# Optimization experiments

Hardware: AMD Instinct MI355X
Metric: run time of the kernel (lower is better)

The kernel has to match this reference:

```python
import jax, jax.numpy as jnp
import numpy as np

MEM = 2048

def _linear_params(key, scale):
    kw, kb = jax.random.split(key)
    W = jax.random.uniform(kw, (MEM, MEM), jnp.float32, -scale, scale)
    b = jax.random.uniform(kb, (MEM,), jnp.float32, -scale, scale)
    return W, b

def setup_inputs() -> dict:
    key = jax.random.key(0)
    ks = jax.random.split(key, 18)
    scale = 1.0 / np.sqrt(MEM)
    inp = {
        'lc': jax.random.normal(ks[0], (1, MEM), jnp.float32),
        'lh': jax.random.normal(ks[1], (1, MEM), jnp.float32),
        'rc': jax.random.normal(ks[2], (1, MEM), jnp.float32),
        'rh': jax.random.normal(ks[3], (1, MEM), jnp.float32),
        'S': jax.random.normal(ks[4], (1, MEM), jnp.float32),
        'w': jax.random.normal(ks[5], (1, MEM), jnp.float32),
    }
    names = ['Wh', 'Us', 'ma', 'ilh', 'irh', 'lflh', 'lfrh', 'rflh', 'rfrh', 'ulh', 'urh']
    for i, n in enumerate(names):
        W, b = _linear_params(ks[6 + i], scale)
        inp[n + '_w'] = W
        inp[n + '_b'] = b
    return inp

def _lin(x, W, b):
    return x @ W.T + b

def reference(lc, lh, rc, rh, S, w,
              Wh_w, Wh_b, Us_w, Us_b, ma_w, ma_b,
              ilh_w, ilh_b, irh_w, irh_b,
              lflh_w, lflh_b, lfrh_w, lfrh_b,
              rflh_w, rflh_b, rfrh_w, rfrh_b,
              ulh_w, ulh_b, urh_w, urh_b):
    # attention scoring over the two children
    m_left = jnp.tanh(_lin(lh, Wh_w, Wh_b) + _lin(S, Us_w, Us_b)).squeeze()   # [MEM]
    m_right = jnp.tanh(_lin(rh, Wh_w, Wh_b) + _lin(S, Us_w, Us_b)).squeeze()  # [MEM]
    exp_left = w @ m_left[:, None]    # [1,1]
    exp_right = w @ m_right[:, None]  # [1,1]
    denom = exp_left + exp_right
    left_alpha = exp_left / denom
    right_alpha = exp_right / denom
    # attention-weighted child hidden states
    la = jnp.tanh(_lin(left_alpha * lh, ma_w, ma_b))   # [1,MEM]
    ra = jnp.tanh(_lin(right_alpha * rh, ma_w, ma_b))  # [1,MEM]
    # tree-LSTM gates
    i = jax.nn.sigmoid(_lin(la, ilh_w, ilh_b) + _lin(ra, irh_w, irh_b))
    lf = jax.nn.sigmoid(_lin(la, lflh_w, lflh_b) + _lin(ra, lfrh_w, lfrh_b))
    rf = jax.nn.sigmoid(_lin(la, rflh_w, rflh_b) + _lin(ra, rfrh_w, rfrh_b))
    update = jnp.tanh(_lin(la, ulh_w, ulh_b) + _lin(ra, urh_w, urh_b))
    c = i * update + lf * lc + rf * rc
    h = jnp.tanh(c)
    return (c, h)
```

## Files before the change

### kernel.cpp

```cpp
#include <hip/hip_runtime.h>
#include <hip/hip_bf16.h>
#include <math.h>

#define MEM 2048
#define NF4 (MEM / 4)

__device__ __forceinline__ float wave_reduce(float v) {
#pragma unroll
    for (int off = 32; off > 0; off >>= 1)
        v += __shfl_down(v, off, 64);
    return v;
}

__device__ __forceinline__ float sigmoidf_(float x) {
    return 1.0f / (1.0f + expf(-x));
}

__global__ __launch_bounds__(256) void
k1_score(const float* __restrict__ lh, const float* __restrict__ rh,
         const float* __restrict__ S,  const float* __restrict__ w,
         const float* __restrict__ Wh_w, const float* __restrict__ Wh_b,
         const float* __restrict__ Us_w, const float* __restrict__ Us_b,
         const float* __restrict__ ma_w,
         float* __restrict__ pl, float* __restrict__ pr,
         float* __restrict__ eacc)
{
    __shared__ __align__(16) float s_lh[MEM];
    __shared__ __align__(16) float s_rh[MEM];
    __shared__ __align__(16) float s_S[MEM];
    __shared__ float s_e[8];

    const int tid = threadIdx.x;
    for (int i = tid; i < MEM; i += 256) {
        s_lh[i] = lh[i];
        s_rh[i] = rh[i];
        s_S[i]  = S[i];
    }
    __syncthreads();

    const int wave = tid >> 6;
    const int lane = tid & 63;
    const int row  = blockIdx.x * 4 + wave;

    const float4* __restrict__ wr = (const float4*)(Wh_w + (size_t)row * MEM);
    const float4* __restrict__ ur = (const float4*)(Us_w + (size_t)row * MEM);
    const float4* __restrict__ mr = (const float4*)(ma_w + (size_t)row * MEM);
    const float4* l4 = (const float4*)s_lh;
    const float4* r4 = (const float4*)s_rh;
    const float4* s4 = (const float4*)s_S;

    float awl = 0.f, awr = 0.f, aus = 0.f, aml = 0.f, amr = 0.f;
#pragma unroll 2
    for (int it = 0; it < NF4 / 64; ++it) {
        const int idx = it * 64 + lane;
        const float4 wv = wr[idx];
        const float4 uv = ur[idx];
        const float4 mv = mr[idx];
        const float4 xl = l4[idx];
        const float4 xr = r4[idx];
        const float4 xs = s4[idx];
        awl += wv.x * xl.x + wv.y * xl.y + wv.z * xl.z + wv.w * xl.w;
        awr += wv.x * xr.x + wv.y * xr.y + wv.z * xr.z + wv.w * xr.w;
        aus += uv.x * xs.x + uv.y * xs.y + uv.z * xs.z + uv.w * xs.w;
        aml += mv.x * xl.x + mv.y * xl.y + mv.z * xl.z + mv.w * xl.w;
        amr += mv.x * xr.x + mv.y * xr.y + mv.z * xr.z + mv.w * xr.w;
    }
    awl = wave_reduce(awl);
    awr = wave_reduce(awr);
    aus = wave_reduce(aus);
    aml = wave_reduce(aml);
    amr = wave_reduce(amr);

    if (lane == 0) {
        const float us = aus + Us_b[row];
        const float ml = tanhf(awl + Wh_b[row] + us);
        const float mrv = tanhf(awr + Wh_b[row] + us);
        pl[row] = aml;
        pr[row] = amr;
        const float wj = w[row];
        s_e[wave]     = wj * ml;
        s_e[4 + wave] = wj * mrv;
    }
    __syncthreads();
    if (tid == 0) {
        atomicAdd(&eacc[0], s_e[0] + s_e[1] + s_e[2] + s_e[3]);
        atomicAdd(&eacc[1], s_e[4] + s_e[5] + s_e[6] + s_e[7]);
    }
}

__global__ __launch_bounds__(256) void
k2_gates(const float* __restrict__ lc, const float* __restrict__ rc,
         const float* __restrict__ pl, const float* __restrict__ pr,
         const float* __restrict__ eacc, const float* __restrict__ ma_b,
         const float* __restrict__ ilh_w,  const float* __restrict__ ilh_b,
         const float* __restrict__ irh_w,  const float* __restrict__ irh_b,
         const float* __restrict__ lflh_w, const float* __restrict__ lflh_b,
         const float* __restrict__ lfrh_w, const float* __restrict__ lfrh_b,
         const float* __restrict__ rflh_w, const float* __restrict__ rflh_b,
         const float* __restrict__ rfrh_w, const float* __restrict__ rfrh_b,
         const float* __restrict__ ulh_w,  const float* __restrict__ ulh_b,
         const float* __restrict__ urh_w,  const float* __restrict__ urh_b,
         float* __restrict__ out)
{
    __shared__ __align__(16) float s_la[MEM];
    __shared__ __align__(16) float s_ra[MEM];

    const int tid = threadIdx.x;
    const float el = eacc[0];
    const float er = eacc[1];
    const float denom = el + er;
    const float al = el / denom;
    const float ar = er / denom;

    for (int i = tid; i < MEM; i += 256) {
        const float mb = ma_b[i];
        s_la[i] = tanhf(al * pl[i] + mb);
        s_ra[i] = tanhf(ar * pr[i] + mb);
    }
    __syncthreads();

    const int wave = tid >> 6;
    const int lane = tid & 63;
    const int row  = blockIdx.x * 4 + wave;
    const size_t off = (size_t)row * MEM;

    const float4* __restrict__ il4  = (const float4*)(ilh_w  + off);
    const float4* __restrict__ ir4  = (const float4*)(irh_w  + off);
    const float4* __restrict__ lfl4 = (const float4*)(lflh_w + off);
    const float4* __restrict__ lfr4 = (const float4*)(lfrh_w + off);
    const float4* __restrict__ rfl4 = (const float4*)(rflh_w + off);
    const float4* __restrict__ rfr4 = (const float4*)(rfrh_w + off);
    const float4* __restrict__ ul4  = (const float4*)(ulh_w  + off);
    const float4* __restrict__ ur4  = (const float4*)(urh_w  + off);
    const float4* la4 = (const float4*)s_la;
    const float4* ra4 = (const float4*)s_ra;

    float ai = 0.f, bi = 0.f, alf = 0.f, blf = 0.f;
    float arf = 0.f, brf = 0.f, au = 0.f, bu = 0.f;
#pragma unroll 2
    for (int it = 0; it < NF4 / 64; ++it) {
        const int idx = it * 64 + lane;
        const float4 xa = la4[idx];
        const float4 xb = ra4[idx];
        float4 v;
        v = il4[idx];  ai  += v.x * xa.x + v.y * xa.y + v.z * xa.z + v.w * xa.w;
        v = ir4[idx];  bi  += v.x * xb.x + v.y * xb.y + v.z * xb.z + v.w * xb.w;
        v = lfl4[idx]; alf += v.x * xa.x + v.y * xa.y + v.z * xa.z + v.w * xa.w;
        v = lfr4[idx]; blf += v.x * xb.x + v.y * xb.y + v.z * xb.z + v.w * xb.w;
        v = rfl4[idx]; arf += v.x * xa.x + v.y * xa.y + v.z * xa.z + v.w * xa.w;
        v = rfr4[idx]; brf += v.x * xb.x + v.y * xb.y + v.z * xb.z + v.w * xb.w;
        v = ul4[idx];  au  += v.x * xa.x + v.y * xa.y + v.z * xa.z + v.w * xa.w;
        v = ur4[idx];  bu  += v.x * xb.x + v.y * xb.y + v.z * xb.z + v.w * xb.w;
    }

    const float gi  = wave_reduce(ai + bi);
    const float glf = wave_reduce(alf + blf);
    const float grf = wave_reduce(arf + brf);
    const float gu  = wave_reduce(au + bu);

    if (lane == 0) {
        const float ig  = sigmoidf_(gi  + ilh_b[row]  + irh_b[row]);
        const float lfg = sigmoidf_(glf + lflh_b[row] + lfrh_b[row]);
        const float rfg = sigmoidf_(grf + rflh_b[row] + rfrh_b[row]);
        const float ug  = tanhf(gu + ulh_b[row] + urh_b[row]);
        const float c = ig * ug + lfg * lc[row] + rfg * rc[row];
        out[row]       = c;
        out[MEM + row] = tanhf(c);
    }
}

extern "C" void kernel_launch(void* const* d_in, const int* in_sizes, int n_in,
                              void* d_out, int out_size, void* d_ws, size_t ws_size,
                              hipStream_t stream) {
    const float* lc = (const float*)d_in[0];
    const float* lh = (const float*)d_in[1];
    const float* rc = (const float*)d_in[2];
    const float* rh = (const float*)d_in[3];
    const float* S  = (const float*)d_in[4];
    const float* w  = (const float*)d_in[5];
    const float* Wh_w   = (const float*)d_in[6];   const float* Wh_b   = (const float*)d_in[7];
    const float* Us_w   = (const float*)d_in[8];   const float* Us_b   = (const float*)d_in[9];
    const float* ma_w   = (const float*)d_in[10];  const float* ma_b   = (const float*)d_in[11];
    const float* ilh_w  = (const float*)d_in[12];  const float* ilh_b  = (const float*)d_in[13];
    const float* irh_w  = (const float*)d_in[14];  const float* irh_b  = (const float*)d_in[15];
    const float* lflh_w = (const float*)d_in[16];  const float* lflh_b = (const float*)d_in[17];
    const float* lfrh_w = (const float*)d_in[18];  const float* lfrh_b = (const float*)d_in[19];
    const float* rflh_w = (const float*)d_in[20];  const float* rflh_b = (const float*)d_in[21];
    const float* rfrh_w = (const float*)d_in[22];  const float* rfrh_b = (const float*)d_in[23];
    const float* ulh_w  = (const float*)d_in[24];  const float* ulh_b  = (const float*)d_in[25];
    const float* urh_w  = (const float*)d_in[26];  const float* urh_b  = (const float*)d_in[27];

    float* out  = (float*)d_out;
    float* ws   = (float*)d_ws;
    float* eacc = ws;
    float* pl   = ws + 64;
    float* pr   = ws + 64 + MEM;

    hipMemsetAsync(eacc, 0, 2 * sizeof(float), stream);

    k1_score<<<MEM / 4, 256, 0, stream>>>(lh, rh, S, w, Wh_w, Wh_b, Us_w, Us_b,
                                          ma_w, pl, pr, eacc);

    k2_gates<<<MEM / 4, 256, 0, stream>>>(lc, rc, pl, pr, eacc, ma_b,
                                          ilh_w, ilh_b, irh_w, irh_b,
                                          lflh_w, lflh_b, lfrh_w, lfrh_b,
                                          rflh_w, rflh_b, rfrh_w, rfrh_b,
                                          ulh_w, ulh_b, urh_w, urh_b, out);
}
```

Before: 261.1 us.

## Use one block per row and replace atomics with per-row score buffers

Each weight row is now handled by a whole 256-thread block, up from one wave per row, and the launch uses 2048 blocks. The first kernel no longer stages the input vectors in shared memory and reads them straight from global/L2. Instead of accumulating attention scores with atomics after a memset, it writes per-row w*m values to a buffer. The second kernel reduces that buffer at the start of every block. This removes the memset launch and the atomic contention, and raises the number of in-flight memory requests for the bandwidth-bound GEMVs. The cost is redundant score reductions and tanh recomputation in every block, plus extra block-level reductions.

```diff
diff --git a/kernel.cpp b/kernel.cpp
--- a/kernel.cpp
+++ b/kernel.cpp
@@ -3,7 +3,12 @@
 #include <math.h>
 
 #define MEM 2048
+#define NT  256
 #define NF4 (MEM / 4)
+
+__device__ __forceinline__ float dot4(float4 a, float4 b) {
+    return a.x * b.x + a.y * b.y + a.z * b.z + a.w * b.w;
+}
 
 __device__ __forceinline__ float wave_reduce(float v) {
 #pragma unroll
@@ -16,54 +21,42 @@
     return 1.0f / (1.0f + expf(-x));
 }
 
-__global__ __launch_bounds__(256) void
+__global__ __launch_bounds__(NT) void
 k1_score(const float* __restrict__ lh, const float* __restrict__ rh,
          const float* __restrict__ S,  const float* __restrict__ w,
          const float* __restrict__ Wh_w, const float* __restrict__ Wh_b,
          const float* __restrict__ Us_w, const float* __restrict__ Us_b,
          const float* __restrict__ ma_w,
          float* __restrict__ pl, float* __restrict__ pr,
-         float* __restrict__ eacc)
+         float* __restrict__ wml, float* __restrict__ wmr)
 {
-    __shared__ __align__(16) float s_lh[MEM];
-    __shared__ __align__(16) float s_rh[MEM];
-    __shared__ __align__(16) float s_S[MEM];
-    __shared__ float s_e[8];
-
-    const int tid = threadIdx.x;
-    for (int i = tid; i < MEM; i += 256) {
-        s_lh[i] = lh[i];
-        s_rh[i] = rh[i];
-        s_S[i]  = S[i];
-    }
-    __syncthreads();
-
-    const int wave = tid >> 6;
-    const int lane = tid & 63;
-    const int row  = blockIdx.x * 4 + wave;
-
-    const float4* __restrict__ wr = (const float4*)(Wh_w + (size_t)row * MEM);
-    const float4* __restrict__ ur = (const float4*)(Us_w + (size_t)row * MEM);
-    const float4* __restrict__ mr = (const float4*)(ma_w + (size_t)row * MEM);
-    const float4* l4 = (const float4*)s_lh;
-    const float4* r4 = (const float4*)s_rh;
-    const float4* s4 = (const float4*)s_S;
+    __shared__ float s_red[4][5];
+
+    const int t   = threadIdx.x;
+    const int row = blockIdx.x;
+
+    const float4* __restrict__ wh4 = (const float4*)(Wh_w + (size_t)row * MEM);
+    const float4* __restrict__ us4 = (const float4*)(Us_w + (size_t)row * MEM);
+    const float4* __restrict__ ma4 = (const float4*)(ma_w + (size_t)row * MEM);
+    const float4* __restrict__ l4  = (const float4*)lh;
+    const float4* __restrict__ r4  = (const float4*)rh;
+    const float4* __restrict__ s4  = (const float4*)S;
 
     float awl = 0.f, awr = 0.f, aus = 0.f, aml = 0.f, amr = 0.f;
-#pragma unroll 2
-    for (int it = 0; it < NF4 / 64; ++it) {
-        const int idx = it * 64 + lane;
-        const float4 wv = wr[idx];
-        const float4 uv = ur[idx];
-        const float4 mv = mr[idx];
-        const float4 xl = l4[idx];
-        const float4 xr = r4[idx];
-        const float4 xs = s4[idx];
-        awl += wv.x * xl.x + wv.y * xl.y + wv.z * xl.z + wv.w * xl.w;
-        awr += wv.x * xr.x + wv.y * xr.y + wv.z * xr.z + wv.w * xr.w;
-        aus += uv.x * xs.x + uv.y * xs.y + uv.z * xs.z + uv.w * xs.w;
-        aml += mv.x * xl.x + mv.y * xl.y + mv.z * xl.z + mv.w * xl.w;
-        amr += mv.x * xr.x + mv.y * xr.y + mv.z * xr.z + mv.w * xr.w;
+#pragma unroll
+    for (int h = 0; h < 2; ++h) {
+        const int i = t + h * NT;
+        const float4 a  = wh4[i];
+        const float4 u  = us4[i];
+        const float4 m  = ma4[i];
+        const float4 xl = l4[i];
+        const float4 xr = r4[i];
+        const float4 xs = s4[i];
+        awl += dot4(a, xl);
+        awr += dot4(a, xr);
+        aus += dot4(u, xs);
+        aml += dot4(m, xl);
+        amr += dot4(m, xr);
     }
     awl = wave_reduce(awl);
     awr = wave_reduce(awr);
@@ -71,27 +64,35 @@
     aml = wave_reduce(aml);
     amr = wave_reduce(amr);
 
-    if (lane == 0) {
-        const float us = aus + Us_b[row];
-        const float ml = tanhf(awl + Wh_b[row] + us);
-        const float mrv = tanhf(awr + Wh_b[row] + us);
-        pl[row] = aml;
-        pr[row] = amr;
+    const int wv = t >> 6, ln = t & 63;
+    if (ln == 0) {
+        s_red[wv][0] = awl; s_red[wv][1] = awr; s_red[wv][2] = aus;
+        s_red[wv][3] = aml; s_red[wv][4] = amr;
+    }
+    __syncthreads();
+    if (t == 0) {
+        float r0 = 0.f, r1 = 0.f, r2 = 0.f, r3 = 0.f, r4v = 0.f;
+#pragma unroll
+        for (int k = 0; k < 4; ++k) {
+            r0 += s_red[k][0]; r1 += s_red[k][1]; r2 += s_red[k][2];
+            r3 += s_red[k][3]; r4v += s_red[k][4];
+        }
+        const float us = r2 + Us_b[row];
+        const float ml = tanhf(r0 + Wh_b[row] + us);
+        const float mr = tanhf(r1 + Wh_b[row] + us);
+        pl[row] = r3;
+        pr[row] = r4v;
         const float wj = w[row];
-        s_e[wave]     = wj * ml;
-        s_e[4 + wave] = wj * mrv;
-    }
-    __syncthreads();
-    if (tid == 0) {
-        atomicAdd(&eacc[0], s_e[0] + s_e[1] + s_e[2] + s_e[3]);
-        atomicAdd(&eacc[1], s_e[4] + s_e[5] + s_e[6] + s_e[7]);
-    }
-}
-
-__global__ __launch_bounds__(256) void
+        wml[row] = wj * ml;
+        wmr[row] = wj * mr;
+    }
+}
+
+__global__ __launch_bounds__(NT) void
 k2_gates(const float* __restrict__ lc, const float* __restrict__ rc,
          const float* __restrict__ pl, const float* __restrict__ pr,
-         const float* __restrict__ eacc, const float* __restrict__ ma_b,
+         const float* __restrict__ wml, const float* __restrict__ wmr,
+         const float* __restrict__ ma_b,
          const float* __restrict__ ilh_w,  const float* __restrict__ ilh_b,
          const float* __restrict__ irh_w,  const float* __restrict__ irh_b,
          const float* __restrict__ lflh_w, const float* __restrict__ lflh_b,
@@ -104,26 +105,60 @@
 {
     __shared__ __align__(16) float s_la[MEM];
     __shared__ __align__(16) float s_ra[MEM];
-
-    const int tid = threadIdx.x;
-    const float el = eacc[0];
-    const float er = eacc[1];
-    const float denom = el + er;
-    const float al = el / denom;
-    const float ar = er / denom;
-
-    for (int i = tid; i < MEM; i += 256) {
-        const float mb = ma_b[i];
-        s_la[i] = tanhf(al * pl[i] + mb);
-        s_ra[i] = tanhf(ar * pr[i] + mb);
-    }
-    __syncthreads();
-
-    const int wave = tid >> 6;
-    const int lane = tid & 63;
-    const int row  = blockIdx.x * 4 + wave;
+    __shared__ float s_red[4][4];
+    __shared__ float s_al[2];
+
+    const int t   = threadIdx.x;
+    const int wv  = t >> 6, ln = t & 63;
+    const int row = blockIdx.x;
+
+    {
+        const float4* __restrict__ wl4 = (const float4*)wml;
+        const float4* __restrict__ wr4 = (const float4*)wmr;
+        const float4 a0 = wl4[t], a1 = wl4[t + NT];
+        const float4 b0 = wr4[t], b1 = wr4[t + NT];
+        float el = a0.x + a0.y + a0.z + a0.w + a1.x + a1.y + a1.z + a1.w;
+        float er = b0.x + b0.y + b0.z + b0.w + b1.x + b1.y + b1.z + b1.w;
+        el = wave_reduce(el);
+        er = wave_reduce(er);
+        if (ln == 0) { s_red[wv][0] = el; s_red[wv][1] = er; }
+    }
+    __syncthreads();
+    if (t == 0) {
+        const float el = s_red[0][0] + s_red[1][0] + s_red[2][0] + s_red[3][0];
+        const float er = s_red[0][1] + s_red[1][1] + s_red[2][1] + s_red[3][1];
+        const float d  = el + er;
+        s_al[0] = el / d;
+        s_al[1] = er / d;
+    }
+    __syncthreads();
+    const float al = s_al[0];
+    const float ar = s_al[1];
+
+    {
+        const float4* __restrict__ p4 = (const float4*)pl;
+        const float4* __restrict__ q4 = (const float4*)pr;
+        const float4* __restrict__ b4 = (const float4*)ma_b;
+        float4* sla4 = (float4*)s_la;
+        float4* sra4 = (float4*)s_ra;
+#pragma unroll
+        for (int h = 0; h < 2; ++h) {
+            const int i = t + h * NT;
+            const float4 p = p4[i];
+            const float4 q = q4[i];
+            const float4 b = b4[i];
+            float4 la, ra;
+            la.x = tanhf(al * p.x + b.x); ra.x = tanhf(ar * q.x + b.x);
+            la.y = tanhf(al * p.y + b.y); ra.y = tanhf(ar * q.y + b.y);
+            la.z = tanhf(al * p.z + b.z); ra.z = tanhf(ar * q.z + b.z);
+            la.w = tanhf(al * p.w + b.w); ra.w = tanhf(ar * q.w + b.w);
+            sla4[i] = la;
+            sra4[i] = ra;
+        }
+    }
+    __syncthreads();
+
     const size_t off = (size_t)row * MEM;
-
     const float4* __restrict__ il4  = (const float4*)(ilh_w  + off);
     const float4* __restrict__ ir4  = (const float4*)(irh_w  + off);
     const float4* __restrict__ lfl4 = (const float4*)(lflh_w + off);
@@ -132,38 +167,48 @@
     const float4* __restrict__ rfr4 = (const float4*)(rfrh_w + off);
     const float4* __restrict__ ul4  = (const float4*)(ulh_w  + off);
     const float4* __restrict__ ur4  = (const float4*)(urh_w  + off);
-    const float4* la4 = (const float4*)s_la;
-    const float4* ra4 = (const float4*)s_ra;
-
-    float ai = 0.f, bi = 0.f, alf = 0.f, blf = 0.f;
-    float arf = 0.f, brf = 0.f, au = 0.f, bu = 0.f;
-#pragma unroll 2
-    for (int it = 0; it < NF4 / 64; ++it) {
-        const int idx = it * 64 + lane;
-        const float4 xa = la4[idx];
-        const float4 xb = ra4[idx];
-        float4 v;
-        v = il4[idx];  ai  += v.x * xa.x + v.y * xa.y + v.z * xa.z + v.w * xa.w;
-        v = ir4[idx];  bi  += v.x * xb.x + v.y * xb.y + v.z * xb.z + v.w * xb.w;
-        v = lfl4[idx]; alf += v.x * xa.x + v.y * xa.y + v.z * xa.z + v.w * xa.w;
-        v = lfr4[idx]; blf += v.x * xb.x + v.y * xb.y + v.z * xb.z + v.w * xb.w;
-        v = rfl4[idx]; arf += v.x * xa.x + v.y * xa.y + v.z * xa.z + v.w * xa.w;
-        v = rfr4[idx]; brf += v.x * xb.x + v.y * xb.y + v.z * xb.z + v.w * xb.w;
-        v = ul4[idx];  au  += v.x * xa.x + v.y * xa.y + v.z * xa.z + v.w * xa.w;
-        v = ur4[idx];  bu  += v.x * xb.x + v.y * xb.y + v.z * xb.z + v.w * xb.w;
-    }
-
-    const float gi  = wave_reduce(ai + bi);
-    const float glf = wave_reduce(alf + blf);
-    const float grf = wave_reduce(arf + brf);
-    const float gu  = wave_reduce(au + bu);
-
-    if (lane == 0) {
-        const float ig  = sigmoidf_(gi  + ilh_b[row]  + irh_b[row]);
-        const float lfg = sigmoidf_(glf + lflh_b[row] + lfrh_b[row]);
-        const float rfg = sigmoidf_(grf + rflh_b[row] + rfrh_b[row]);
-        const float ug  = tanhf(gu + ulh_b[row] + urh_b[row]);
-        const float c = ig * ug + lfg * lc[row] + rfg * rc[row];
+    const float4* sla4 = (const float4*)s_la;
+    const float4* sra4 = (const float4*)s_ra;
+
+    float gi = 0.f, glf = 0.f, grf = 0.f, gu = 0.f;
+#pragma unroll
+    for (int h = 0; h < 2; ++h) {
+        const int i = t + h * NT;
+        const float4 w0 = il4[i];
+        const float4 w1 = ir4[i];
+        const float4 w2 = lfl4[i];
+        const float4 w3 = lfr4[i];
+        const float4 w4 = rfl4[i];
+        const float4 w5 = rfr4[i];
+        const float4 w6 = ul4[i];
+        const float4 w7 = ur4[i];
+        const float4 xa = sla4[i];
+        const float4 xb = sra4[i];
+        gi  += dot4(w0, xa) + dot4(w1, xb);
+        glf += dot4(w2, xa) + dot4(w3, xb);
+        grf += dot4(w4, xa) + dot4(w5, xb);
+        gu  += dot4(w6, xa) + dot4(w7, xb);
+    }
+    gi  = wave_reduce(gi);
+    glf = wave_reduce(glf);
+    grf = wave_reduce(grf);
+    gu  = wave_reduce(gu);
+    if (ln == 0) {
+        s_red[wv][0] = gi; s_red[wv][1] = glf; s_red[wv][2] = grf; s_red[wv][3] = gu;
+    }
+    __syncthreads();
+    if (t == 0) {
+        float r0 = 0.f, r1 = 0.f, r2 = 0.f, r3 = 0.f;
+#pragma unroll
+        for (int k = 0; k < 4; ++k) {
+            r0 += s_red[k][0]; r1 += s_red[k][1];
+            r2 += s_red[k][2]; r3 += s_red[k][3];
+        }
+        const float ig  = sigmoidf_(r0 + ilh_b[row]  + irh_b[row]);
+        const float lfg = sigmoidf_(r1 + lflh_b[row] + lfrh_b[row]);
+        const float rfg = sigmoidf_(r2 + rflh_b[row] + rfrh_b[row]);
+        const float ug  = tanhf(r3 + ulh_b[row] + urh_b[row]);
+        const float c   = ig * ug + lfg * lc[row] + rfg * rc[row];
         out[row]       = c;
         out[MEM + row] = tanhf(c);
     }
@@ -190,20 +235,19 @@
     const float* ulh_w  = (const float*)d_in[24];  const float* ulh_b  = (const float*)d_in[25];
     const float* urh_w  = (const float*)d_in[26];  const float* urh_b  = (const float*)d_in[27];
 
-    float* out  = (float*)d_out;
-    float* ws   = (float*)d_ws;
-    float* eacc = ws;
-    float* pl   = ws + 64;
-    float* pr   = ws + 64 + MEM;
-
-    hipMemsetAsync(eacc, 0, 2 * sizeof(float), stream);
-
-    k1_score<<<MEM / 4, 256, 0, stream>>>(lh, rh, S, w, Wh_w, Wh_b, Us_w, Us_b,
-                                          ma_w, pl, pr, eacc);
-
-    k2_gates<<<MEM / 4, 256, 0, stream>>>(lc, rc, pl, pr, eacc, ma_b,
-                                          ilh_w, ilh_b, irh_w, irh_b,
-                                          lflh_w, lflh_b, lfrh_w, lfrh_b,
-                                          rflh_w, rflh_b, rfrh_w, rfrh_b,
-                                          ulh_w, ulh_b, urh_w, urh_b, out);
-}
+    float* out = (float*)d_out;
+    float* ws  = (float*)d_ws;
+    float* pl  = ws;
+    float* pr  = ws + MEM;
+    float* wml = ws + 2 * MEM;
+    float* wmr = ws + 3 * MEM;
+
+    k1_score<<<MEM, NT, 0, stream>>>(lh, rh, S, w, Wh_w, Wh_b, Us_w, Us_b,
+                                     ma_w, pl, pr, wml, wmr);
+
+    k2_gates<<<MEM, NT, 0, stream>>>(lc, rc, pl, pr, wml, wmr, ma_b,
+                                     ilh_w, ilh_b, irh_w, irh_b,
+                                     lflh_w, lflh_b, lfrh_w, lfrh_b,
+                                     rflh_w, rflh_b, rfrh_w, rfrh_b,
+                                     ulh_w, ulh_b, urh_w, urh_b, out);
+}
```

Result: faster. 244.0 us (-6.6%).
